# Kernel tuning notes

Hardware: AMD Instinct MI355X
Metric: run time of the kernel (lower is better)

The kernel has to match this reference:

```python
import jax, jax.numpy as jnp
import numpy as np

HEADS = 16
EPS = 1e-5

def _ln(x, g, b):
    m = jnp.mean(x, axis=-1, keepdims=True)
    v = jnp.mean((x - m) ** 2, axis=-1, keepdims=True)
    return (x - m) * jax.lax.rsqrt(v + EPS) * g + b

def setup_inputs() -> dict:
    key = jax.random.key(0)
    ks = jax.random.split(key, 12)
    B, N, C, H = 4, 2048, 1024, 4096
    d = {}
    d['x'] = jax.random.normal(ks[0], (B, N, C), jnp.float32)
    d['pos_embed'] = jax.random.normal(ks[1], (1, N, C), jnp.float32)
    # LayerNorm params (normq, normk, normv, norm)
    for nm in ['nq', 'nk', 'nv', 'n']:
        d[nm + '_g'] = jnp.ones((C,), jnp.float32)
        d[nm + '_b'] = jnp.zeros((C,), jnp.float32)
    s = 1.0 / np.sqrt(C)
    d['wq'] = jax.random.uniform(ks[2], (C, C), jnp.float32, -s, s)
    d['bq'] = jnp.zeros((C,), jnp.float32)
    d['wk'] = jax.random.uniform(ks[3], (C, C), jnp.float32, -s, s)
    d['bk'] = jnp.zeros((C,), jnp.float32)
    d['wv'] = jax.random.uniform(ks[4], (C, C), jnp.float32, -s, s)
    d['bv'] = jnp.zeros((C,), jnp.float32)
    d['wp'] = jax.random.uniform(ks[5], (C, C), jnp.float32, -s, s)
    d['bp'] = jnp.zeros((C,), jnp.float32)
    d['w1'] = jax.random.uniform(ks[6], (C, H), jnp.float32, -s, s)
    d['b1'] = jnp.zeros((H,), jnp.float32)
    sh = 1.0 / np.sqrt(H)
    d['w2'] = jax.random.uniform(ks[7], (H, C), jnp.float32, -sh, sh)
    d['b2'] = jnp.zeros((C,), jnp.float32)
    return d

def reference(x, pos_embed, nq_g, nq_b, nk_g, nk_b, nv_g, nv_b, wq, bq, wk, bk, wv, bv, wp, bp, n_g, n_b, w1, b1, w2, b2):
    B, N, C = x.shape
    hd = C // HEADS
    scale = hd ** -0.5
    q_in = x
    k_in = x + pos_embed
    v_in = x + pos_embed
    # Attention (eval mode: dropout = identity)
    q = (_ln(q_in, nq_g, nq_b) @ wq + bq).reshape(B, N, HEADS, hd)
    k = (_ln(k_in, nk_g, nk_b) @ wk + bk).reshape(B, N, HEADS, hd)
    v = (_ln(v_in, nv_g, nv_b) @ wv + bv).reshape(B, N, HEADS, hd)
    attn = jnp.einsum('bqhd,bkhd->bhqk', q, k) * scale
    attn = jax.nn.softmax(attn, axis=-1)
    out = jnp.einsum('bhqk,bkhd->bqhd', attn, v).reshape(B, N, C)
    out = out @ wp + bp
    # residual + MLP
    h = q_in + out
    y = _ln(h, n_g, n_b) @ w1 + b1
    y = jnp.where(y >= 0, y, 0.1 * y)  # LeakyReLU(0.1)
    y = y @ w2 + b2
    return h + y
```

## Files before the change

kernel.cpp:

```cpp
#include <hip/hip_runtime.h>
#include <hip/hip_bf16.h>

#define DEV __device__ __forceinline__

typedef __attribute__((ext_vector_type(8))) short short8;
typedef __attribute__((ext_vector_type(4))) short short4v;
typedef __attribute__((ext_vector_type(4))) float f32x4;
typedef __attribute__((ext_vector_type(2))) int int2v;

constexpr int Bb   = 4;
constexpr int SEQ  = 2048;
constexpr int C    = 1024;
constexpr int HID  = 4096;
constexpr int NH   = 16;
constexpr int HD   = 64;
constexpr int MTOT = Bb * SEQ;

DEV unsigned bfbits(float f) {
  unsigned x = __float_as_uint(f);
  return (x + 0x7fffu + ((x >> 16) & 1u)) >> 16;
}

DEV short f2bf(float f) { return (short)bfbits(f); }

DEV unsigned packrn(float a, float b) {
  unsigned ua = __float_as_uint(a) + 0x8000u;
  unsigned ub = __float_as_uint(b) + 0x8000u;
  return __builtin_amdgcn_perm(ub, ua, 0x07060302u);
}

DEV float fexp2(float x) {
#if __has_builtin(__builtin_amdgcn_exp2f)
  return __builtin_amdgcn_exp2f(x);
#else
  float r;
  asm("v_exp_f32 %0, %1" : "=v"(r) : "v"(x));
  return r;
#endif
}

DEV void gload16(const void* g, void* l) {
  __builtin_amdgcn_global_load_lds((const __attribute__((address_space(1))) void*)g,
                                   (__attribute__((address_space(3))) void*)l, 16, 0, 0);
}

DEV f32x4 mfma16(short4v a, short4v b, f32x4 c) {
#if __has_builtin(__builtin_amdgcn_mfma_f32_16x16x16bf16_1k)
  return __builtin_amdgcn_mfma_f32_16x16x16bf16_1k(a, b, c, 0, 0, 0);
#else
  asm volatile("v_mfma_f32_16x16x16_bf16 %0, %1, %2, %0" : "+v"(c) : "v"(a), "v"(b));
  return c;
#endif
}

DEV void transpose_body(const float* __restrict__ src, short* __restrict__ dst,
                        int R, int Cc) {
  __shared__ float t[32][33];
  int tx = threadIdx.x & 31, ty = threadIdx.x >> 5;
  int c0 = blockIdx.x * 32, r0 = blockIdx.y * 32;
  #pragma unroll
  for (int i = 0; i < 4; i++)
    t[ty + i * 8][tx] = src[(size_t)(r0 + ty + i * 8) * Cc + c0 + tx];
  __syncthreads();
  #pragma unroll
  for (int i = 0; i < 4; i++)
    dst[(size_t)(c0 + ty + i * 8) * R + r0 + tx] = f2bf(t[tx][ty + i * 8]);
}

__global__ void k_transpose_w(const float* __restrict__ src, short* __restrict__ dst,
                              int R, int Cc) {
  transpose_body(src, dst, R, Cc);
}

__global__ void k_transpose_w4(const float* __restrict__ s0, const float* __restrict__ s1,
                               const float* __restrict__ s2, const float* __restrict__ s3,
                               short* __restrict__ d0, short* __restrict__ d1,
                               short* __restrict__ d2, short* __restrict__ d3) {
  const float* s = blockIdx.z == 0 ? s0 : blockIdx.z == 1 ? s1 : blockIdx.z == 2 ? s2 : s3;
  short*       d = blockIdx.z == 0 ? d0 : blockIdx.z == 1 ? d1 : blockIdx.z == 2 ? d2 : d3;
  transpose_body(s, d, C, C);
}

__global__ void k_transpose_v(const short* __restrict__ V, short* __restrict__ Vt) {
  __shared__ short t[32][33];
  int tx = threadIdx.x & 31, ty = threadIdx.x >> 5;
  int plane = blockIdx.z;
  int b = plane >> 4, h = plane & 15;
  int n0 = blockIdx.x * 32, d0 = blockIdx.y * 32;
  #pragma unroll
  for (int i = 0; i < 4; i++)
    t[ty + i * 8][tx] = V[(size_t)(b * SEQ + n0 + ty + i * 8) * C + h * HD + d0 + tx];
  __syncthreads();
  #pragma unroll
  for (int i = 0; i < 4; i++)
    Vt[((size_t)plane * HD + d0 + ty + i * 8) * SEQ + n0 + tx] = t[tx][ty + i * 8];
}

__global__ void k_ln_qkv(const float* __restrict__ x, const float* __restrict__ pos,
                         const float* __restrict__ nqg, const float* __restrict__ nqb,
                         const float* __restrict__ nkg, const float* __restrict__ nkb,
                         const float* __restrict__ nvg, const float* __restrict__ nvb,
                         short* __restrict__ xq, short* __restrict__ xk,
                         short* __restrict__ xv) {
  int row = blockIdx.x, tid = threadIdx.x;
  int n = row & (SEQ - 1);
  float a4[4], p4[4];
  float s1 = 0, s2 = 0, t1 = 0, t2 = 0;
  #pragma unroll
  for (int i = 0; i < 4; i++) {
    int c = tid + i * 256;
    float a = x[(size_t)row * C + c];
    float p = pos[(size_t)n * C + c] + a;
    a4[i] = a; p4[i] = p;
    s1 += a; s2 += a * a; t1 += p; t2 += p * p;
  }
  #pragma unroll
  for (int off = 32; off; off >>= 1) {
    s1 += __shfl_xor(s1, off, 64);
    s2 += __shfl_xor(s2, off, 64);
    t1 += __shfl_xor(t1, off, 64);
    t2 += __shfl_xor(t2, off, 64);
  }
  __shared__ float red[4][4];
  int wave = tid >> 6, lane = tid & 63;
  if (lane == 0) { red[wave][0] = s1; red[wave][1] = s2; red[wave][2] = t1; red[wave][3] = t2; }
  __syncthreads();
  s1 = red[0][0] + red[1][0] + red[2][0] + red[3][0];
  s2 = red[0][1] + red[1][1] + red[2][1] + red[3][1];
  t1 = red[0][2] + red[1][2] + red[2][2] + red[3][2];
  t2 = red[0][3] + red[1][3] + red[2][3] + red[3][3];
  float mq = s1 * (1.f / C), mk = t1 * (1.f / C);
  float rq = rsqrtf(s2 * (1.f / C) - mq * mq + 1e-5f);
  float rk = rsqrtf(t2 * (1.f / C) - mk * mk + 1e-5f);
  #pragma unroll
  for (int i = 0; i < 4; i++) {
    int c = tid + i * 256;
    float nq_ = (a4[i] - mq) * rq;
    float nk_ = (p4[i] - mk) * rk;
    xq[(size_t)row * C + c] = f2bf(nq_ * nqg[c] + nqb[c]);
    xk[(size_t)row * C + c] = f2bf(nk_ * nkg[c] + nkb[c]);
    xv[(size_t)row * C + c] = f2bf(nk_ * nvg[c] + nvb[c]);
  }
}

__global__ void k_ln1(const float* __restrict__ h, const float* __restrict__ g,
                      const float* __restrict__ bta, short* __restrict__ out) {
  int row = blockIdx.x, tid = threadIdx.x;
  float a4[4];
  float s1 = 0, s2 = 0;
  #pragma unroll
  for (int i = 0; i < 4; i++) {
    int c = tid + i * 256;
    float a = h[(size_t)row * C + c];
    a4[i] = a; s1 += a; s2 += a * a;
  }
  #pragma unroll
  for (int off = 32; off; off >>= 1) {
    s1 += __shfl_xor(s1, off, 64);
    s2 += __shfl_xor(s2, off, 64);
  }
  __shared__ float red[4][2];
  int wave = tid >> 6, lane = tid & 63;
  if (lane == 0) { red[wave][0] = s1; red[wave][1] = s2; }
  __syncthreads();
  s1 = red[0][0] + red[1][0] + red[2][0] + red[3][0];
  s2 = red[0][1] + red[1][1] + red[2][1] + red[3][1];
  float m = s1 * (1.f / C);
  float r = rsqrtf(s2 * (1.f / C) - m * m + 1e-5f);
  #pragma unroll
  for (int i = 0; i < 4; i++) {
    int c = tid + i * 256;
    out[(size_t)row * C + c] = f2bf((a4[i] - m) * r * g[c] + bta[c]);
  }
}

template <typename EPI>
DEV void gemm_body(const short* __restrict__ A, const short* __restrict__ Bt,
                   int Kk, short* sA, short* sB, EPI&& epi) {
  const int tid = threadIdx.x;
  const int wave = tid >> 6, lane = tid & 63, quad = lane >> 4, l15 = lane & 15;
  const int wm = (wave >> 1) * 64, wn = (wave & 1) * 64;
  constexpr int BO = 128 * 32;

  const int r0 = tid >> 2, s0 = (tid & 3) * 8;
  const short* gA0 = A + (size_t)r0 * Kk + s0;
  const short* gA1 = A + (size_t)(r0 + 64) * Kk + s0;
  const short* gB0 = Bt + (size_t)r0 * Kk + s0;
  const short* gB1 = Bt + (size_t)(r0 + 64) * Kk + s0;
  short* lA0 = &sA[tid * 8];
  short* lA1 = &sA[(tid + 256) * 8];
  short* lB0 = &sB[tid * 8];
  short* lB1 = &sB[(tid + 256) * 8];

  const f32x4 fzero = {0.f, 0.f, 0.f, 0.f};
  f32x4 acc[4][4];
  #pragma unroll
  for (int mi = 0; mi < 4; mi++)
    #pragma unroll
    for (int ni = 0; ni < 4; ni++) acc[mi][ni] = fzero;

  gload16(gA0, lA0);
  gload16(gA1, lA1);
  gload16(gB0, lB0);
  gload16(gB1, lB1);

  for (int k0 = 0; k0 < Kk; k0 += 32) {
    const int buf = (k0 >> 5) & 1;
    __syncthreads();
    if (k0 + 32 < Kk) {
      const int bo = (buf ^ 1) * BO;
      gload16(gA0 + k0 + 32, lA0 + bo);
      gload16(gA1 + k0 + 32, lA1 + bo);
      gload16(gB0 + k0 + 32, lB0 + bo);
      gload16(gB1 + k0 + 32, lB1 + bo);
    }
    const int bo = buf * BO;
    short8 av[4], bv[4];
    #pragma unroll
    for (int mi = 0; mi < 4; mi++)
      av[mi] = *(const short8*)&sA[bo + (wm + mi * 16 + l15) * 32 + quad * 8];
    #pragma unroll
    for (int ni = 0; ni < 4; ni++)
      bv[ni] = *(const short8*)&sB[bo + (wn + ni * 16 + l15) * 32 + quad * 8];
    #pragma unroll
    for (int mi = 0; mi < 4; mi++)
      #pragma unroll
      for (int ni = 0; ni < 4; ni++)
        acc[mi][ni] = __builtin_amdgcn_mfma_f32_16x16x32_bf16(av[mi], bv[ni], acc[mi][ni], 0, 0, 0);
  }
  epi(acc, wm, wn, quad, l15);
}

template <int MODE>
__global__ __launch_bounds__(256, 2)
void k_gemm(const short* __restrict__ A, const short* __restrict__ Bt,
            const float* __restrict__ bias, const float* __restrict__ resid,
            void* __restrict__ outp, int Nn, int Kk) {
  __shared__ short sA[2 * 128 * 32];
  __shared__ short sB[2 * 128 * 32];
  const int m0 = blockIdx.x * 128, n0 = blockIdx.y * 128;
  gemm_body(A + (size_t)m0 * Kk, Bt + (size_t)n0 * Kk, Kk, sA, sB,
    [&](f32x4 (&acc)[4][4], int wm, int wn, int quad, int l15) {
      float bb[4];
      #pragma unroll
      for (int ni = 0; ni < 4; ni++) bb[ni] = bias[n0 + wn + ni * 16 + l15];
      #pragma unroll
      for (int mi = 0; mi < 4; mi++) {
        #pragma unroll
        for (int ni = 0; ni < 4; ni++) {
          #pragma unroll
          for (int r = 0; r < 4; r++) {
            int row = m0 + wm + mi * 16 + quad * 4 + r;
            int col = n0 + wn + ni * 16 + l15;
            float v = acc[mi][ni][r] + bb[ni];
            if constexpr (MODE == 1) v = v >= 0.f ? v : 0.1f * v;
            if constexpr (MODE == 2)
              ((float*)outp)[(size_t)row * Nn + col] = resid[(size_t)row * Nn + col] + v;
            else
              ((short*)outp)[(size_t)row * Nn + col] = f2bf(v);
          }
        }
      }
    });
}

template <int Q>
DEV void phase8(const short* __restrict__ sAb, const short* __restrict__ sBb,
                f32x4 (&acc)[4][4], int wm, int wn, int quad, int l15) {
  constexpr int mis = (Q & 1) * 2, nis = (Q >> 1) * 2;
  short8 av[2][2], bv[2][2];
  #pragma unroll
  for (int m2 = 0; m2 < 2; m2++) {
    const int rA = wm + (mis + m2) * 16 + l15;
    const int sw = rA & 7;
    #pragma unroll
    for (int ks = 0; ks < 2; ks++)
      av[m2][ks] = *(const short8*)&sAb[rA * 64 + ((ks * 4 + quad) ^ sw) * 8];
  }
  #pragma unroll
  for (int n2 = 0; n2 < 2; n2++) {
    const int rB = wn + (nis + n2) * 16 + l15;
    const int sw = rB & 7;
    #pragma unroll
    for (int ks = 0; ks < 2; ks++)
      bv[n2][ks] = *(const short8*)&sBb[rB * 64 + ((ks * 4 + quad) ^ sw) * 8];
  }
  __builtin_amdgcn_s_barrier();
  asm volatile("s_waitcnt lgkmcnt(0)" ::: "memory");
  __builtin_amdgcn_sched_barrier(0);
  __builtin_amdgcn_s_setprio(1);
  #pragma unroll
  for (int ks = 0; ks < 2; ks++)
    #pragma unroll
    for (int m2 = 0; m2 < 2; m2++)
      #pragma unroll
      for (int n2 = 0; n2 < 2; n2++)
        acc[mis + m2][nis + n2] = __builtin_amdgcn_mfma_f32_16x16x32_bf16(
            av[m2][ks], bv[n2][ks], acc[mis + m2][nis + n2], 0, 0, 0);
  __builtin_amdgcn_s_setprio(0);
  __builtin_amdgcn_s_barrier();
}

template <int MODE>
__global__ __launch_bounds__(512, 1)
void k_gemm8(const short* __restrict__ A, const short* __restrict__ Bt,
             const float* __restrict__ bias, const float* __restrict__ resid,
             void* __restrict__ outp, int Nn, int Kk) {
  __shared__ __align__(16) short sA[2][128 * 64];
  __shared__ __align__(16) short sB[2][256 * 64];
  const int tid = threadIdx.x;
  const int wave = tid >> 6, lane = tid & 63, quad = lane >> 4, l15 = lane & 15;
  const int wm = (wave >> 2) * 64, wn = (wave & 3) * 64;

  const int gx = gridDim.x;
  const int nwg = gx * gridDim.y;
  const int orig = blockIdx.y * gx + blockIdx.x;
  const int swz = (orig & 7) * (nwg >> 3) + (orig >> 3);
  const int m0 = (swz % gx) * 128, n0 = (swz / gx) * 256;

  const int sr = tid >> 3, su = tid & 7;
  const int sx = (su ^ (sr & 7)) * 8;
  const short* gA0 = A + (size_t)(m0 + sr) * Kk + sx;
  const short* gA1 = gA0 + (size_t)64 * Kk;
  const short* gB0 = Bt + (size_t)(n0 + sr) * Kk + sx;
  const short* gB1 = gB0 + (size_t)64 * Kk;
  const short* gB2 = gB0 + (size_t)128 * Kk;
  const short* gB3 = gB0 + (size_t)192 * Kk;

  auto stg = [&](int t) {
    const int b_ = t & 1, ko = t << 6;
    gload16(gA0 + ko, &sA[b_][(size_t)tid * 8]);
    gload16(gA1 + ko, &sA[b_][(size_t)(512 + tid) * 8]);
    gload16(gB0 + ko, &sB[b_][(size_t)tid * 8]);
    gload16(gB1 + ko, &sB[b_][(size_t)(512 + tid) * 8]);
    gload16(gB2 + ko, &sB[b_][(size_t)(1024 + tid) * 8]);
    gload16(gB3 + ko, &sB[b_][(size_t)(1536 + tid) * 8]);
  };

  const f32x4 fzero = {0.f, 0.f, 0.f, 0.f};
  f32x4 acc[4][4];
  #pragma unroll
  for (int mi = 0; mi < 4; mi++)
    #pragma unroll
    for (int ni = 0; ni < 4; ni++) acc[mi][ni] = fzero;

  const int nkt = Kk >> 6;
  stg(0);
  for (int t = 0; t < nkt; t += 2) {
    if (t + 1 < nkt) { stg(t + 1); asm volatile("s_waitcnt vmcnt(6)" ::: "memory"); }
    else             {             asm volatile("s_waitcnt vmcnt(0)" ::: "memory"); }
    __builtin_amdgcn_s_barrier();
    {
      const short* a_ = &sA[t & 1][0]; const short* b_ = &sB[t & 1][0];
      phase8<0>(a_, b_, acc, wm, wn, quad, l15);
      phase8<1>(a_, b_, acc, wm, wn, quad, l15);
      phase8<2>(a_, b_, acc, wm, wn, quad, l15);
      phase8<3>(a_, b_, acc, wm, wn, quad, l15);
    }
    if (t + 1 >= nkt) break;
    if (t + 2 < nkt) { stg(t + 2); asm volatile("s_waitcnt vmcnt(6)" ::: "memory"); }
    else             {             asm volatile("s_waitcnt vmcnt(0)" ::: "memory"); }
    __builtin_amdgcn_s_barrier();
    {
      const short* a_ = &sA[(t + 1) & 1][0]; const short* b_ = &sB[(t + 1) & 1][0];
      phase8<0>(a_, b_, acc, wm, wn, quad, l15);
      phase8<1>(a_, b_, acc, wm, wn, quad, l15);
      phase8<2>(a_, b_, acc, wm, wn, quad, l15);
      phase8<3>(a_, b_, acc, wm, wn, quad, l15);
    }
  }

  float bb[4];
  #pragma unroll
  for (int ni = 0; ni < 4; ni++) bb[ni] = bias[n0 + wn + ni * 16 + l15];
  #pragma unroll
  for (int mi = 0; mi < 4; mi++) {
    #pragma unroll
    for (int ni = 0; ni < 4; ni++) {
      #pragma unroll
      for (int r = 0; r < 4; r++) {
        int row = m0 + wm + mi * 16 + quad * 4 + r;
        int col = n0 + wn + ni * 16 + l15;
        float v = acc[mi][ni][r] + bb[ni];
        if constexpr (MODE == 1) v = v >= 0.f ? v : 0.1f * v;
        if constexpr (MODE == 2)
          ((float*)outp)[(size_t)row * Nn + col] = resid[(size_t)row * Nn + col] + v;
        else
          ((short*)outp)[(size_t)row * Nn + col] = f2bf(v);
      }
    }
  }
}

__global__ __launch_bounds__(256, 2)
void k_gemm_qkv(const short* __restrict__ xq, const short* __restrict__ xk,
                const short* __restrict__ xv,
                const short* __restrict__ wqT, const short* __restrict__ wkT,
                const short* __restrict__ wvT,
                const float* __restrict__ bq, const float* __restrict__ bk,
                const float* __restrict__ bv,
                short* __restrict__ Qm, short* __restrict__ Km, short* __restrict__ Vm) {
  __shared__ short sA[2 * 128 * 32];
  __shared__ short sB[2 * 128 * 32];
  const int z = blockIdx.z;
  const short* A    = z == 0 ? xq : z == 1 ? xk : xv;
  const short* Bt   = z == 0 ? wqT : z == 1 ? wkT : wvT;
  const float* bias = z == 0 ? bq : z == 1 ? bk : bv;
  short* outp       = z == 0 ? Qm : z == 1 ? Km : Vm;
  const float scale = z == 0 ? 0.1803368801111244f : 1.0f;
  const int m0 = blockIdx.x * 128, n0 = blockIdx.y * 128;
  gemm_body(A + (size_t)m0 * C, Bt + (size_t)n0 * C, C, sA, sB,
    [&](f32x4 (&acc)[4][4], int wm, int wn, int quad, int l15) {
      float bb[4];
      #pragma unroll
      for (int ni = 0; ni < 4; ni++) bb[ni] = bias[n0 + wn + ni * 16 + l15];
      #pragma unroll
      for (int mi = 0; mi < 4; mi++)
        #pragma unroll
        for (int ni = 0; ni < 4; ni++)
          #pragma unroll
          for (int r = 0; r < 4; r++) {
            int row = m0 + wm + mi * 16 + quad * 4 + r;
            int col = n0 + wn + ni * 16 + l15;
            outp[(size_t)row * C + col] = f2bf((acc[mi][ni][r] + bb[ni]) * scale);
          }
    });
}

__global__ __launch_bounds__(256, 4)
void k_attn(const short* __restrict__ Q, const short* __restrict__ K,
            const short* __restrict__ Vt, short* __restrict__ O) {
  __shared__ __align__(16) short sK[2][64 * 64];
  __shared__ __align__(16) short sV[2][64 * 64];
  const int tid = threadIdx.x;
  const int bh = blockIdx.x;
  const int b = bh >> 4, h = bh & 15;
  const int q0 = blockIdx.y * 128;
  const int wave = tid >> 6, lane = tid & 63, quad = lane >> 4, l15 = lane & 15;
  const int wm = wave * 32;
  const size_t tokBase = (size_t)b * SEQ;

  short8 qf[2][2];
  #pragma unroll
  for (int qi = 0; qi < 2; qi++)
    #pragma unroll
    for (int hf = 0; hf < 2; hf++)
      qf[qi][hf] = *(const short8*)(Q + (tokBase + q0 + wm + qi * 16 + l15) * C
                                    + h * HD + hf * 32 + quad * 8);

  const int r0 = tid >> 3,        c0s = ((tid & 7) ^ (r0 & 7)) * 8;
  const int r1 = (tid + 256) >> 3, c1s = ((tid & 7) ^ (r1 & 7)) * 8;
  const short* gK0 = K + (tokBase + r0) * C + h * HD + c0s;
  const short* gK1 = K + (tokBase + r1) * C + h * HD + c1s;
  const short* gV0 = Vt + ((size_t)bh * HD + r0) * SEQ + c0s;
  const short* gV1 = Vt + ((size_t)bh * HD + r1) * SEQ + c1s;
  short* lK0 = &sK[0][tid * 8];
  short* lK1 = &sK[0][(tid + 256) * 8];
  short* lV0 = &sV[0][tid * 8];
  short* lV1 = &sV[0][(tid + 256) * 8];
  constexpr int BUFO = 64 * 64;

#define STAGE(bufsel, kb) {                                   \
    int kk = (kb) * 64, bo = (bufsel) * BUFO;                 \
    gload16(gK0 + (size_t)kk * C, lK0 + bo);                  \
    gload16(gK1 + (size_t)kk * C, lK1 + bo);                  \
    gload16(gV0 + kk,             lV0 + bo);                  \
    gload16(gV1 + kk,             lV1 + bo); }

  const f32x4 fzero = {0.f, 0.f, 0.f, 0.f};
  const short4v onesv = {0x3F80, 0x3F80, 0x3F80, 0x3F80};
  f32x4 o[2][4];
  f32x4 oSum[2] = {fzero, fzero};
  #pragma unroll
  for (int qi = 0; qi < 2; qi++)
    #pragma unroll
    for (int di = 0; di < 4; di++) o[qi][di] = fzero;

  const int sw = l15 & 7;

  STAGE(0, 0)

  for (int kb = 0; kb < SEQ / 64; kb++) {
    const int buf = kb & 1;
    __syncthreads();
    if (kb + 1 < SEQ / 64) STAGE(buf ^ 1, kb + 1)

    unsigned pk[4][2][2];
    #pragma unroll
    for (int ki = 0; ki < 4; ki++) {
      const int krow = (ki * 16 + l15) * 64;
      short8 a0 = *(const short8*)&sK[buf][krow + ((0 + quad) ^ sw) * 8];
      short8 a1 = *(const short8*)&sK[buf][krow + ((4 + quad) ^ sw) * 8];
      #pragma unroll
      for (int qi = 0; qi < 2; qi++) {
        f32x4 st = __builtin_amdgcn_mfma_f32_16x16x32_bf16(a0, qf[qi][0], fzero, 0, 0, 0);
        st = __builtin_amdgcn_mfma_f32_16x16x32_bf16(a1, qf[qi][1], st, 0, 0, 0);
        float p0 = fexp2(st[0]), p1 = fexp2(st[1]);
        float p2 = fexp2(st[2]), p3 = fexp2(st[3]);
        pk[ki][qi][0] = packrn(p0, p1);
        pk[ki][qi][1] = packrn(p2, p3);
      }
    }

    #pragma unroll
    for (int ki = 0; ki < 4; ki++) {
      short4v bv[4];
      const int g = ((ki * 2 + (quad >> 1)) ^ sw) * 8 + (quad & 1) * 4;
      #pragma unroll
      for (int di = 0; di < 4; di++)
        bv[di] = *(const short4v*)&sV[buf][(di * 16 + l15) * 64 + g];
      #pragma unroll
      for (int qi = 0; qi < 2; qi++) {
        int2v t; t.x = (int)pk[ki][qi][0]; t.y = (int)pk[ki][qi][1];
        short4v aP = __builtin_bit_cast(short4v, t);
        oSum[qi] = mfma16(aP, onesv, oSum[qi]);
        #pragma unroll
        for (int di = 0; di < 4; di++)
          o[qi][di] = mfma16(aP, bv[di], o[qi][di]);
      }
    }
  }
#undef STAGE

  float linv[2][4];
  #pragma unroll
  for (int qi = 0; qi < 2; qi++)
    #pragma unroll
    for (int r = 0; r < 4; r++)
      linv[qi][r] = 1.0f / oSum[qi][r];

  #pragma unroll
  for (int qi = 0; qi < 2; qi++)
    #pragma unroll
    for (int di = 0; di < 4; di++)
      #pragma unroll
      for (int r = 0; r < 4; r++) {
        int row = q0 + wm + qi * 16 + quad * 4 + r;
        int col = h * HD + di * 16 + l15;
        O[(tokBase + row) * C + col] = f2bf(o[qi][di][r] * linv[qi][r]);
      }
}

extern "C" void kernel_launch(void* const* d_in, const int* in_sizes, int n_in,
                              void* d_out, int out_size, void* d_ws, size_t ws_size,
                              hipStream_t stream) {
  const float* x   = (const float*)d_in[0];
  const float* pos = (const float*)d_in[1];
  const float* nqg = (const float*)d_in[2];
  const float* nqb = (const float*)d_in[3];
  const float* nkg = (const float*)d_in[4];
  const float* nkb = (const float*)d_in[5];
  const float* nvg = (const float*)d_in[6];
  const float* nvb = (const float*)d_in[7];
  const float* ng  = (const float*)d_in[8];
  const float* nb  = (const float*)d_in[9];
  const float* wq  = (const float*)d_in[10];
  const float* bq  = (const float*)d_in[11];
  const float* wk  = (const float*)d_in[12];
  const float* bk  = (const float*)d_in[13];
  const float* wv  = (const float*)d_in[14];
  const float* bv  = (const float*)d_in[15];
  const float* wp  = (const float*)d_in[16];
  const float* bp  = (const float*)d_in[17];
  const float* w1  = (const float*)d_in[18];
  const float* b1  = (const float*)d_in[19];
  const float* w2  = (const float*)d_in[20];
  const float* b2  = (const float*)d_in[21];

  char* ws = (char*)d_ws;
  const size_t MB = 1u << 20;
  short* wqT  = (short*)(ws + 0 * MB);
  short* wkT  = (short*)(ws + 2 * MB);
  short* wvT  = (short*)(ws + 4 * MB);
  short* wpT  = (short*)(ws + 6 * MB);
  short* w1T  = (short*)(ws + 8 * MB);
  short* w2T  = (short*)(ws + 16 * MB);
  short* xq   = (short*)(ws + 24 * MB);
  short* xk   = (short*)(ws + 40 * MB);
  short* xv   = (short*)(ws + 56 * MB);
  short* Qm   = (short*)(ws + 72 * MB);
  short* Km   = (short*)(ws + 88 * MB);
  short* Vm   = (short*)(ws + 104 * MB);
  short* Vt   = (short*)(ws + 120 * MB);
  short* y1   = (short*)(ws + 72 * MB);
  short* Ob   = xk;
  short* hln  = xq;
  float* hbuf = (float*)(ws + 136 * MB);
  (void)ws_size; (void)in_sizes; (void)n_in; (void)out_size;

  dim3 blk(256);
  k_transpose_w4<<<dim3(32, 32, 4), blk, 0, stream>>>(wq, wk, wv, wp, wqT, wkT, wvT, wpT);
  k_transpose_w<<<dim3(128, 32), blk, 0, stream>>>(w1, w1T, C, HID);
  k_transpose_w<<<dim3(32, 128), blk, 0, stream>>>(w2, w2T, HID, C);
  k_ln_qkv<<<dim3(MTOT), blk, 0, stream>>>(x, pos, nqg, nqb, nkg, nkb, nvg, nvb, xq, xk, xv);
  k_gemm_qkv<<<dim3(MTOT / 128, C / 128, 3), blk, 0, stream>>>(xq, xk, xv, wqT, wkT, wvT,
                                                               bq, bk, bv, Qm, Km, Vm);
  k_transpose_v<<<dim3(SEQ / 32, HD / 32, Bb * NH), blk, 0, stream>>>(Vm, Vt);
  k_attn<<<dim3(Bb * NH, SEQ / 128), blk, 0, stream>>>(Qm, Km, Vt, Ob);
  k_gemm<2><<<dim3(MTOT / 128, C / 128), blk, 0, stream>>>(Ob, wpT, bp, x, hbuf, C, C);
  k_ln1<<<dim3(MTOT), blk, 0, stream>>>(hbuf, ng, nb, hln);
  k_gemm<1><<<dim3(MTOT / 128, HID / 128), blk, 0, stream>>>(hln, w1T, b1, nullptr, y1, HID, C);
  k_gemm8<2><<<dim3(MTOT / 128, C / 256), dim3(512), 0, stream>>>(y1, w2T, b2, hbuf,
                                                                  (float*)d_out, C, HID);
}
```

Baseline: 566.2 us.

## Triple-buffer GEMM LDS tiles and interleave prefetch with two half-tile MFMA phases

The bf16 GEMM kernel moves from double to triple LDS buffering, so global loads for tile t+2 are issued while tile t is being computed. Those loads are split into two halves, each issued inside one of two MFMA phases. Each phase now covers all four M sub-tiles against half of the N sub-tiles, instead of the previous four quarter phases. The workgroup-order swizzle is removed in favour of direct blockIdx mapping, which may reduce L2 reuse, and the larger LDS footprint leaves less headroom. An unused lambda is left in the code.

```diff
diff --git a/kernel.cpp b/kernel.cpp
--- a/kernel.cpp
+++ b/kernel.cpp
@@ -264,59 +264,17 @@
     });
 }
 
-template <int Q>
-DEV void phase8(const short* __restrict__ sAb, const short* __restrict__ sBb,
-                f32x4 (&acc)[4][4], int wm, int wn, int quad, int l15) {
-  constexpr int mis = (Q & 1) * 2, nis = (Q >> 1) * 2;
-  short8 av[2][2], bv[2][2];
-  #pragma unroll
-  for (int m2 = 0; m2 < 2; m2++) {
-    const int rA = wm + (mis + m2) * 16 + l15;
-    const int sw = rA & 7;
-    #pragma unroll
-    for (int ks = 0; ks < 2; ks++)
-      av[m2][ks] = *(const short8*)&sAb[rA * 64 + ((ks * 4 + quad) ^ sw) * 8];
-  }
-  #pragma unroll
-  for (int n2 = 0; n2 < 2; n2++) {
-    const int rB = wn + (nis + n2) * 16 + l15;
-    const int sw = rB & 7;
-    #pragma unroll
-    for (int ks = 0; ks < 2; ks++)
-      bv[n2][ks] = *(const short8*)&sBb[rB * 64 + ((ks * 4 + quad) ^ sw) * 8];
-  }
-  __builtin_amdgcn_s_barrier();
-  asm volatile("s_waitcnt lgkmcnt(0)" ::: "memory");
-  __builtin_amdgcn_sched_barrier(0);
-  __builtin_amdgcn_s_setprio(1);
-  #pragma unroll
-  for (int ks = 0; ks < 2; ks++)
-    #pragma unroll
-    for (int m2 = 0; m2 < 2; m2++)
-      #pragma unroll
-      for (int n2 = 0; n2 < 2; n2++)
-        acc[mis + m2][nis + n2] = __builtin_amdgcn_mfma_f32_16x16x32_bf16(
-            av[m2][ks], bv[n2][ks], acc[mis + m2][nis + n2], 0, 0, 0);
-  __builtin_amdgcn_s_setprio(0);
-  __builtin_amdgcn_s_barrier();
-}
-
 template <int MODE>
 __global__ __launch_bounds__(512, 1)
 void k_gemm8(const short* __restrict__ A, const short* __restrict__ Bt,
              const float* __restrict__ bias, const float* __restrict__ resid,
              void* __restrict__ outp, int Nn, int Kk) {
-  __shared__ __align__(16) short sA[2][128 * 64];
-  __shared__ __align__(16) short sB[2][256 * 64];
+  __shared__ __align__(16) short sA[3][128 * 64];
+  __shared__ __align__(16) short sB[3][256 * 64];
   const int tid = threadIdx.x;
   const int wave = tid >> 6, lane = tid & 63, quad = lane >> 4, l15 = lane & 15;
   const int wm = (wave >> 2) * 64, wn = (wave & 3) * 64;
-
-  const int gx = gridDim.x;
-  const int nwg = gx * gridDim.y;
-  const int orig = blockIdx.y * gx + blockIdx.x;
-  const int swz = (orig & 7) * (nwg >> 3) + (orig >> 3);
-  const int m0 = (swz % gx) * 128, n0 = (swz / gx) * 256;
+  const int m0 = blockIdx.x * 128, n0 = blockIdx.y * 256;
 
   const int sr = tid >> 3, su = tid & 7;
   const int sx = (su ^ (sr & 7)) * 8;
@@ -327,8 +285,17 @@
   const short* gB2 = gB0 + (size_t)128 * Kk;
   const short* gB3 = gB0 + (size_t)192 * Kk;
 
+  const f32x4 fzero = {0.f, 0.f, 0.f, 0.f};
+  f32x4 acc[4][4];
+  #pragma unroll
+  for (int mi = 0; mi < 4; mi++)
+    #pragma unroll
+    for (int ni = 0; ni < 4; ni++) acc[mi][ni] = fzero;
+
+  const int nkt = Kk >> 6;
+
   auto stg = [&](int t) {
-    const int b_ = t & 1, ko = t << 6;
+    const int b_ = t % 3, ko = t << 6;
     gload16(gA0 + ko, &sA[b_][(size_t)tid * 8]);
     gload16(gA1 + ko, &sA[b_][(size_t)(512 + tid) * 8]);
     gload16(gB0 + ko, &sB[b_][(size_t)tid * 8]);
@@ -336,37 +303,144 @@
     gload16(gB2 + ko, &sB[b_][(size_t)(1024 + tid) * 8]);
     gload16(gB3 + ko, &sB[b_][(size_t)(1536 + tid) * 8]);
   };
-
-  const f32x4 fzero = {0.f, 0.f, 0.f, 0.f};
-  f32x4 acc[4][4];
-  #pragma unroll
-  for (int mi = 0; mi < 4; mi++)
-    #pragma unroll
-    for (int ni = 0; ni < 4; ni++) acc[mi][ni] = fzero;
-
-  const int nkt = Kk >> 6;
+  auto stgA_ = [&](int t) {
+    const int b_ = t % 3, ko = t << 6;
+    gload16(gA0 + ko, &sA[b_][(size_t)tid * 8]);
+    gload16(gA1 + ko, &sA[b_][(size_t)(512 + tid) * 8]);
+    gload16(gB0 + ko, &sB[b_][(size_t)tid * 8]);
+  };
+  auto stgB_ = [&](int t) {
+    const int b_ = t % 3, ko = t << 6;
+    gload16(gB1 + ko, &sB[b_][(size_t)(512 + tid) * 8]);
+    gload16(gB2 + ko, &sB[b_][(size_t)(1024 + tid) * 8]);
+    gload16(gB3 + ko, &sB[b_][(size_t)(1536 + tid) * 8]);
+  };
+
+  auto phase = [&](const short* sAb, const short* sBb, int HALF) {
+    short8 av[4][2], bv[2][2];
+    #pragma unroll
+    for (int m2 = 0; m2 < 4; m2++) {
+      const int rA = wm + m2 * 16 + l15;
+      const int sw = rA & 7;
+      #pragma unroll
+      for (int ks = 0; ks < 2; ks++)
+        av[m2][ks] = *(const short8*)&sAb[rA * 64 + ((ks * 4 + quad) ^ sw) * 8];
+    }
+    #pragma unroll
+    for (int n2 = 0; n2 < 2; n2++) {
+      const int rB = wn + (HALF * 2 + n2) * 16 + l15;
+      const int sw = rB & 7;
+      #pragma unroll
+      for (int ks = 0; ks < 2; ks++)
+        bv[n2][ks] = *(const short8*)&sBb[rB * 64 + ((ks * 4 + quad) ^ sw) * 8];
+    }
+    return HALF == 0
+      ? (void)0, [&](short8 (&av_)[4][2], short8 (&bv_)[2][2], int H) {
+          __builtin_amdgcn_s_barrier();
+          asm volatile("s_waitcnt lgkmcnt(0)" ::: "memory");
+          __builtin_amdgcn_sched_barrier(0);
+          __builtin_amdgcn_s_setprio(1);
+          #pragma unroll
+          for (int ks = 0; ks < 2; ks++)
+            #pragma unroll
+            for (int m2 = 0; m2 < 4; m2++)
+              #pragma unroll
+              for (int n2 = 0; n2 < 2; n2++)
+                acc[m2][H * 2 + n2] = __builtin_amdgcn_mfma_f32_16x16x32_bf16(
+                    av_[m2][ks], bv_[n2][ks], acc[m2][H * 2 + n2], 0, 0, 0);
+          __builtin_amdgcn_s_setprio(0);
+          __builtin_amdgcn_s_barrier();
+        }(av, bv, HALF)
+      : [&](short8 (&av_)[4][2], short8 (&bv_)[2][2], int H) {
+          __builtin_amdgcn_s_barrier();
+          asm volatile("s_waitcnt lgkmcnt(0)" ::: "memory");
+          __builtin_amdgcn_sched_barrier(0);
+          __builtin_amdgcn_s_setprio(1);
+          #pragma unroll
+          for (int ks = 0; ks < 2; ks++)
+            #pragma unroll
+            for (int m2 = 0; m2 < 4; m2++)
+              #pragma unroll
+              for (int n2 = 0; n2 < 2; n2++)
+                acc[m2][H * 2 + n2] = __builtin_amdgcn_mfma_f32_16x16x32_bf16(
+                    av_[m2][ks], bv_[n2][ks], acc[m2][H * 2 + n2], 0, 0, 0);
+          __builtin_amdgcn_s_setprio(0);
+          __builtin_amdgcn_s_barrier();
+        }(av, bv, HALF);
+  };
+
   stg(0);
-  for (int t = 0; t < nkt; t += 2) {
-    if (t + 1 < nkt) { stg(t + 1); asm volatile("s_waitcnt vmcnt(6)" ::: "memory"); }
-    else             {             asm volatile("s_waitcnt vmcnt(0)" ::: "memory"); }
+  if (nkt > 1) stg(1);
+
+  for (int t = 0; t < nkt; t++) {
+    if (t + 1 < nkt) asm volatile("s_waitcnt vmcnt(6)" ::: "memory");
+    else             asm volatile("s_waitcnt vmcnt(0)" ::: "memory");
     __builtin_amdgcn_s_barrier();
+    const short* a_ = &sA[t % 3][0];
+    const short* b_ = &sB[t % 3][0];
     {
-      const short* a_ = &sA[t & 1][0]; const short* b_ = &sB[t & 1][0];
-      phase8<0>(a_, b_, acc, wm, wn, quad, l15);
-      phase8<1>(a_, b_, acc, wm, wn, quad, l15);
-      phase8<2>(a_, b_, acc, wm, wn, quad, l15);
-      phase8<3>(a_, b_, acc, wm, wn, quad, l15);
-    }
-    if (t + 1 >= nkt) break;
-    if (t + 2 < nkt) { stg(t + 2); asm volatile("s_waitcnt vmcnt(6)" ::: "memory"); }
-    else             {             asm volatile("s_waitcnt vmcnt(0)" ::: "memory"); }
-    __builtin_amdgcn_s_barrier();
+      short8 av[4][2], bv[2][2];
+      #pragma unroll
+      for (int m2 = 0; m2 < 4; m2++) {
+        const int rA = wm + m2 * 16 + l15, sw = rA & 7;
+        #pragma unroll
+        for (int ks = 0; ks < 2; ks++)
+          av[m2][ks] = *(const short8*)&a_[rA * 64 + ((ks * 4 + quad) ^ sw) * 8];
+      }
+      #pragma unroll
+      for (int n2 = 0; n2 < 2; n2++) {
+        const int rB = wn + n2 * 16 + l15, sw = rB & 7;
+        #pragma unroll
+        for (int ks = 0; ks < 2; ks++)
+          bv[n2][ks] = *(const short8*)&b_[rB * 64 + ((ks * 4 + quad) ^ sw) * 8];
+      }
+      if (t + 2 < nkt) stgA_(t + 2);
+      __builtin_amdgcn_s_barrier();
+      asm volatile("s_waitcnt lgkmcnt(0)" ::: "memory");
+      __builtin_amdgcn_sched_barrier(0);
+      __builtin_amdgcn_s_setprio(1);
+      #pragma unroll
+      for (int ks = 0; ks < 2; ks++)
+        #pragma unroll
+        for (int m2 = 0; m2 < 4; m2++)
+          #pragma unroll
+          for (int n2 = 0; n2 < 2; n2++)
+            acc[m2][n2] = __builtin_amdgcn_mfma_f32_16x16x32_bf16(
+                av[m2][ks], bv[n2][ks], acc[m2][n2], 0, 0, 0);
+      __builtin_amdgcn_s_setprio(0);
+      __builtin_amdgcn_s_barrier();
+    }
     {
-      const short* a_ = &sA[(t + 1) & 1][0]; const short* b_ = &sB[(t + 1) & 1][0];
-      phase8<0>(a_, b_, acc, wm, wn, quad, l15);
-      phase8<1>(a_, b_, acc, wm, wn, quad, l15);
-      phase8<2>(a_, b_, acc, wm, wn, quad, l15);
-      phase8<3>(a_, b_, acc, wm, wn, quad, l15);
+      short8 av[4][2], bv[2][2];
+      #pragma unroll
+      for (int m2 = 0; m2 < 4; m2++) {
+        const int rA = wm + m2 * 16 + l15, sw = rA & 7;
+        #pragma unroll
+        for (int ks = 0; ks < 2; ks++)
+          av[m2][ks] = *(const short8*)&a_[rA * 64 + ((ks * 4 + quad) ^ sw) * 8];
+      }
+      #pragma unroll
+      for (int n2 = 0; n2 < 2; n2++) {
+        const int rB = wn + (2 + n2) * 16 + l15, sw = rB & 7;
+        #pragma unroll
+        for (int ks = 0; ks < 2; ks++)
+          bv[n2][ks] = *(const short8*)&b_[rB * 64 + ((ks * 4 + quad) ^ sw) * 8];
+      }
+      if (t + 2 < nkt) stgB_(t + 2);
+      __builtin_amdgcn_s_barrier();
+      asm volatile("s_waitcnt lgkmcnt(0)" ::: "memory");
+      __builtin_amdgcn_sched_barrier(0);
+      __builtin_amdgcn_s_setprio(1);
+      #pragma unroll
+      for (int ks = 0; ks < 2; ks++)
+        #pragma unroll
+        for (int m2 = 0; m2 < 4; m2++)
+          #pragma unroll
+          for (int n2 = 0; n2 < 2; n2++)
+            acc[m2][2 + n2] = __builtin_amdgcn_mfma_f32_16x16x32_bf16(
+                av[m2][ks], bv[n2][ks], acc[m2][2 + n2], 0, 0, 0);
+      __builtin_amdgcn_s_setprio(0);
+      __builtin_amdgcn_s_barrier();
     }
   }
 
```

Result: faster. 540.4 us (-4.6%).
